# Kernel tuning notes

Measured on AMD Instinct MI355X. Metric: run time of the kernel, lower is better.

The kernel has to match this reference:

```python
import jax, jax.numpy as jnp
import numpy as np
from jax import lax

VOCAB = 50257
BEAM = 8
BSZ = 64
STEP = 16
NGRAM = 4
CAND_MULT = 2


def setup_inputs() -> dict:
    key = jax.random.key(0)
    k1, k2, k3 = jax.random.split(key, 3)
    lprobs = jax.random.normal(k1, (BSZ, BEAM, VOCAB), dtype=jnp.float32)
    scores = jax.random.normal(k2, (BSZ, BEAM, STEP), dtype=jnp.float32)
    mask = jax.random.randint(k3, (BSZ, BEAM, NGRAM), 0, 2, dtype=jnp.int32)
    return {"lprobs": lprobs, "scores": scores, "mask": mask, "step": STEP}


def reference(lprobs, scores, mask, step):
    bsz, beam_size, vocab_size = lprobs.shape
    k = CAND_MULT * beam_size

    # mask: (b, beam, n_gram) -> keep beam only if all n_gram entries nonzero
    # (original repeats over vocab then sums; summing first is equivalent and
    # avoids materializing the (b, beam, vocab, n_gram) tensor)
    n_gram = mask.shape[-1]
    keep = jnp.sum(mask, axis=-1) == n_gram  # (b, beam) bool
    lprobs = jnp.where(keep[:, :, None], lprobs, 0.0)

    if step == 0:
        lprobs = lprobs[:, 0:1, :]
        beam_size = 1
    else:
        # broadcast-add previous cumulative score of each beam
        lprobs = lprobs + scores[:, :, step - 1][:, :, None]

    flat = lprobs.reshape(bsz, beam_size * vocab_size)
    scores_buf, indices_flat = lax.top_k(flat, k)  # (b, k)
    beams_buf = indices_flat // vocab_size
    indices_buf = indices_flat % vocab_size
    return scores_buf, indices_buf, beams_buf
```

## Files before the change

### kernel.cpp

```cpp
#include <hip/hip_runtime.h>

#define VOCAB 50257
#define BEAM  8
#define BSZ   64
#define KSEL  16
#define CHUNK 4
#define TPB   256
#define PER   12568
#define BLKS_PER_ROW (BEAM * CHUNK)
#define NCAND (BLKS_PER_ROW * KSEL)
#define CAP   1024
#define SLOTS 13
#define EMPTY_KEY 1ull

static __device__ __forceinline__ unsigned int ord32(float f) {
    unsigned int u = __float_as_uint(f);
    return (u & 0x80000000u) ? ~u : (u | 0x80000000u);
}
static __device__ __forceinline__ float unord32(unsigned int o) {
    unsigned int u = (o & 0x80000000u) ? (o & 0x7FFFFFFFu) : ~o;
    return __uint_as_float(u);
}
static __device__ __forceinline__ unsigned long long mkkey(float v, unsigned int flat) {
    return ((unsigned long long)ord32(v) << 32) | (0xFFFFFFFFu - flat);
}
static __device__ __forceinline__ void publish(unsigned long long* p, unsigned long long k) {
    __hip_atomic_store(p, k, __ATOMIC_RELAXED, __HIP_MEMORY_SCOPE_AGENT);
}
static __device__ __forceinline__ unsigned long long poll(const unsigned long long* p) {
    return __hip_atomic_load(p, __ATOMIC_RELAXED, __HIP_MEMORY_SCOPE_AGENT);
}
static __device__ __forceinline__ bool slot_valid(unsigned long long k) {
    const unsigned int lo = (unsigned int)k;
    return (lo == 1u) || (lo >= 0xFFF00000u);
}

__global__ __launch_bounds__(TPB)
void beam_topk_fused(const float* __restrict__ lprobs,
                     const float* __restrict__ scores,
                     const int*   __restrict__ mask,
                     const int*   __restrict__ stepp,
                     unsigned long long* __restrict__ ws,
                     float* __restrict__ out)
{
    const int blk   = blockIdx.x;
    const int chunk = blk % CHUNK;
    const int beam  = (blk / CHUNK) % BEAM;
    const int b     = blk / (CHUNK * BEAM);
    const int tid   = threadIdx.x;
    const int step  = stepp[0];

    __shared__ unsigned long long tmax[TPB];
    __shared__ unsigned long long cand[CAP];
    __shared__ unsigned long long rowkeys[NCAND];
    __shared__ unsigned long long theta_s;
    __shared__ int ccount;
    __shared__ int wcnt;
    __shared__ int wid[KSEL];

    unsigned long long* okeys = ws + (size_t)blk * KSEL;
    const int  bb   = b * BEAM + beam;
    const int* m    = mask + bb * 4;
    const bool keep = (m[0] + m[1] + m[2] + m[3]) == 4;
    const float sadd  = (step == 0) ? 0.0f : scores[bb * 16 + (step - 1)];
    const bool active = (step != 0) || (beam == 0);
    const bool finisher = (beam == 0) && (chunk == 0);

    if (!active || (!keep && chunk != 0)) {
        if (tid < KSEL) publish(&okeys[tid], EMPTY_KEY);
    } else if (!keep) {
        if (tid < KSEL)
            publish(&okeys[tid], mkkey(sadd, (unsigned)(beam * VOCAB + tid)));
    } else {
        const int lo  = chunk * PER;
        const int len = ((lo + PER < VOCAB) ? PER : (VOCAB - lo));
        const float* base = lprobs + (size_t)bb * VOCAB;
        const float4* base4 = (const float4*)(base + lo);
        const unsigned int fb = (unsigned)(beam * VOCAB + lo);
        const int nv4 = (len + 3) >> 2;

        unsigned long long m0 = 0ull, m1 = 0ull, m2 = 0ull, m3 = 0ull;
        int j = tid;
        for (; j + 3 * TPB < nv4 - 1 || (j + 3 * TPB == nv4 - 1 && (len & 3) == 0);
             j += 4 * TPB) {
            const float4 v0 = base4[j];
            const float4 v1 = base4[j + TPB];
            const float4 v2 = base4[j + 2 * TPB];
            const float4 v3 = base4[j + 3 * TPB];
            unsigned long long k;
            const unsigned e0 = fb + 4u * (unsigned)j;
            const unsigned e1 = fb + 4u * (unsigned)(j + TPB);
            const unsigned e2 = fb + 4u * (unsigned)(j + 2 * TPB);
            const unsigned e3 = fb + 4u * (unsigned)(j + 3 * TPB);
            k = mkkey(v0.x + sadd, e0);     if (k > m0) m0 = k;
            k = mkkey(v0.y + sadd, e0 + 1); if (k > m0) m0 = k;
            k = mkkey(v0.z + sadd, e0 + 2); if (k > m0) m0 = k;
            k = mkkey(v0.w + sadd, e0 + 3); if (k > m0) m0 = k;
            k = mkkey(v1.x + sadd, e1);     if (k > m1) m1 = k;
            k = mkkey(v1.y + sadd, e1 + 1); if (k > m1) m1 = k;
            k = mkkey(v1.z + sadd, e1 + 2); if (k > m1) m1 = k;
            k = mkkey(v1.w + sadd, e1 + 3); if (k > m1) m1 = k;
            k = mkkey(v2.x + sadd, e2);     if (k > m2) m2 = k;
            k = mkkey(v2.y + sadd, e2 + 1); if (k > m2) m2 = k;
            k = mkkey(v2.z + sadd, e2 + 2); if (k > m2) m2 = k;
            k = mkkey(v2.w + sadd, e2 + 3); if (k > m2) m2 = k;
            k = mkkey(v3.x + sadd, e3);     if (k > m3) m3 = k;
            k = mkkey(v3.y + sadd, e3 + 1); if (k > m3) m3 = k;
            k = mkkey(v3.z + sadd, e3 + 2); if (k > m3) m3 = k;
            k = mkkey(v3.w + sadd, e3 + 3); if (k > m3) m3 = k;
        }
        for (; j < nv4; j += TPB) {
            const int e = 4 * j;
            #pragma unroll
            for (int u = 0; u < 4; ++u) {
                if (e + u < len) {
                    const unsigned long long k = mkkey(base[lo + e + u] + sadd,
                                                       fb + (unsigned)(e + u));
                    if (k > m0) m0 = k;
                }
            }
        }
        if (m1 > m0) m0 = m1;
        if (m2 > m0) m0 = m2;
        if (m3 > m0) m0 = m3;
        const unsigned long long mx = m0;

        tmax[tid] = mx;
        if (tid == 0) { ccount = 0; wcnt = 0; }
        __syncthreads();

        int r = 0;
        for (int jj = 0; jj < TPB; ++jj) r += (tmax[jj] > mx) ? 1 : 0;
        if (r == KSEL - 1) theta_s = mx;
        __syncthreads();
        const unsigned long long theta = theta_s;

        if (mx >= theta) wid[atomicAdd(&wcnt, 1)] = tid;
        __syncthreads();

        for (int t = tid; t < KSEL * SLOTS; t += TPB) {
            const int w  = wid[t / SLOTS];
            const int jj = w + (t % SLOTS) * TPB;
            if (jj < nv4) {
                const int e = 4 * jj;
                if (e + 3 < len) {
                    const float4 v = base4[jj];
                    const unsigned eb = fb + (unsigned)e;
                    unsigned long long k;
                    k = mkkey(v.x + sadd, eb);     if (k >= theta) cand[atomicAdd(&ccount,1)] = k;
                    k = mkkey(v.y + sadd, eb + 1); if (k >= theta) cand[atomicAdd(&ccount,1)] = k;
                    k = mkkey(v.z + sadd, eb + 2); if (k >= theta) cand[atomicAdd(&ccount,1)] = k;
                    k = mkkey(v.w + sadd, eb + 3); if (k >= theta) cand[atomicAdd(&ccount,1)] = k;
                } else {
                    #pragma unroll
                    for (int u = 0; u < 4; ++u) {
                        if (e + u < len) {
                            const unsigned long long k =
                                mkkey(base[lo + e + u] + sadd, fb + (unsigned)(e + u));
                            if (k >= theta) cand[atomicAdd(&ccount,1)] = k;
                        }
                    }
                }
            }
        }
        __syncthreads();
        const int n = ccount;

        for (int c = tid; c < n; c += TPB) {
            const unsigned long long k0 = cand[c];
            int rank = 0;
            for (int jj = 0; jj < n; ++jj) rank += (cand[jj] > k0) ? 1 : 0;
            if (rank < KSEL) publish(&okeys[rank], k0);
        }
    }

    if (!finisher) return;

    const unsigned long long* src = ws + (size_t)b * NCAND;
    for (int i = tid; i < NCAND; i += TPB) {
        unsigned long long k;
        for (;;) {
            k = poll(&src[i]);
            if (slot_valid(k)) break;
            __builtin_amdgcn_s_sleep(2);
        }
        rowkeys[i] = k;
    }
    __syncthreads();
    if (tid == 0) ccount = 0;
    __syncthreads();

    for (int i = tid; i < NCAND; i += TPB) {
        const unsigned long long k = rowkeys[i];
        if ((unsigned int)(k >> 32) != 0u) cand[atomicAdd(&ccount, 1)] = k;
    }
    __syncthreads();
    const int n = ccount;

    for (int c = tid; c < n; c += TPB) {
        const unsigned long long k0 = cand[c];
        int rank = 0;
        for (int jj = 0; jj < n; ++jj) rank += (cand[jj] > k0) ? 1 : 0;
        if (rank < KSEL) {
            const unsigned int flat = 0xFFFFFFFFu - (unsigned int)(k0 & 0xFFFFFFFFull);
            const float val = unord32((unsigned int)(k0 >> 32));
            const int vi = (int)(flat % VOCAB);
            const int bi = (int)(flat / VOCAB);
            out[b * KSEL + rank]                  = val;
            out[BSZ * KSEL + b * KSEL + rank]     = (float)vi;
            out[2 * BSZ * KSEL + b * KSEL + rank] = (float)bi;
        }
    }
}

extern "C" void kernel_launch(void* const* d_in, const int* in_sizes, int n_in,
                              void* d_out, int out_size, void* d_ws, size_t ws_size,
                              hipStream_t stream)
{
    const float* lprobs = (const float*)d_in[0];
    const float* scores = (const float*)d_in[1];
    const int*   mask   = (const int*)d_in[2];
    const int*   stepp  = (const int*)d_in[3];
    float* out = (float*)d_out;
    unsigned long long* ws = (unsigned long long*)d_ws;

    hipLaunchKernelGGL(beam_topk_fused, dim3(BSZ * BEAM * CHUNK), dim3(TPB), 0, stream,
                       lprobs, scores, mask, stepp, ws, out);
}
```

Baseline: 145.5 us.

## Halve block size and fully unroll per-thread max scan with float compares

Cuts threads per block from 256 to 128 and scales the second-pass slot count and candidate capacity to match. The max-finding pass now issues all 24 float4 loads at once, then does cheap float compares that track only a local index, and builds the 64-bit key four times at the end instead of once per element. The aim is more memory-level parallelism and less 64-bit integer work in the hot loop. In exchange it raises register pressure (24 float4 values live at once) and doubles the serial work each thread does in the rank and candidate stages.

Measured after the change: 144.0 us. No clear change (-1.0%).

```diff
diff --git a/kernel.cpp b/kernel.cpp
--- a/kernel.cpp
+++ b/kernel.cpp
@@ -5,12 +5,12 @@
 #define BSZ   64
 #define KSEL  16
 #define CHUNK 4
-#define TPB   256
+#define TPB   128
 #define PER   12568
 #define BLKS_PER_ROW (BEAM * CHUNK)
 #define NCAND (BLKS_PER_ROW * KSEL)
-#define CAP   1024
-#define SLOTS 13
+#define SLOTS 25
+#define CAP   1600
 #define EMPTY_KEY 1ull
 
 static __device__ __forceinline__ unsigned int ord32(float f) {
@@ -35,7 +35,7 @@
     return (lo == 1u) || (lo >= 0xFFF00000u);
 }
 
-__global__ __launch_bounds__(TPB)
+__global__ __launch_bounds__(TPB, 4)
 void beam_topk_fused(const float* __restrict__ lprobs,
                      const float* __restrict__ scores,
                      const int*   __restrict__ mask,
@@ -79,57 +79,71 @@
         const unsigned int fb = (unsigned)(beam * VOCAB + lo);
         const int nv4 = (len + 3) >> 2;
 
-        unsigned long long m0 = 0ull, m1 = 0ull, m2 = 0ull, m3 = 0ull;
-        int j = tid;
-        for (; j + 3 * TPB < nv4 - 1 || (j + 3 * TPB == nv4 - 1 && (len & 3) == 0);
-             j += 4 * TPB) {
-            const float4 v0 = base4[j];
-            const float4 v1 = base4[j + TPB];
-            const float4 v2 = base4[j + 2 * TPB];
-            const float4 v3 = base4[j + 3 * TPB];
-            unsigned long long k;
-            const unsigned e0 = fb + 4u * (unsigned)j;
-            const unsigned e1 = fb + 4u * (unsigned)(j + TPB);
-            const unsigned e2 = fb + 4u * (unsigned)(j + 2 * TPB);
-            const unsigned e3 = fb + 4u * (unsigned)(j + 3 * TPB);
-            k = mkkey(v0.x + sadd, e0);     if (k > m0) m0 = k;
-            k = mkkey(v0.y + sadd, e0 + 1); if (k > m0) m0 = k;
-            k = mkkey(v0.z + sadd, e0 + 2); if (k > m0) m0 = k;
-            k = mkkey(v0.w + sadd, e0 + 3); if (k > m0) m0 = k;
-            k = mkkey(v1.x + sadd, e1);     if (k > m1) m1 = k;
-            k = mkkey(v1.y + sadd, e1 + 1); if (k > m1) m1 = k;
-            k = mkkey(v1.z + sadd, e1 + 2); if (k > m1) m1 = k;
-            k = mkkey(v1.w + sadd, e1 + 3); if (k > m1) m1 = k;
-            k = mkkey(v2.x + sadd, e2);     if (k > m2) m2 = k;
-            k = mkkey(v2.y + sadd, e2 + 1); if (k > m2) m2 = k;
-            k = mkkey(v2.z + sadd, e2 + 2); if (k > m2) m2 = k;
-            k = mkkey(v2.w + sadd, e2 + 3); if (k > m2) m2 = k;
-            k = mkkey(v3.x + sadd, e3);     if (k > m3) m3 = k;
-            k = mkkey(v3.y + sadd, e3 + 1); if (k > m3) m3 = k;
-            k = mkkey(v3.z + sadd, e3 + 2); if (k > m3) m3 = k;
-            k = mkkey(v3.w + sadd, e3 + 3); if (k > m3) m3 = k;
-        }
-        for (; j < nv4; j += TPB) {
-            const int e = 4 * j;
-            #pragma unroll
-            for (int u = 0; u < 4; ++u) {
-                if (e + u < len) {
-                    const unsigned long long k = mkkey(base[lo + e + u] + sadd,
-                                                       fb + (unsigned)(e + u));
-                    if (k > m0) m0 = k;
+        float af0 = -INFINITY, af1 = -INFINITY, af2 = -INFINITY, af3 = -INFINITY;
+        int   ac0 = 0, ac1 = 0, ac2 = 0, ac3 = 0;
+
+#define LD(s) const float4 v##s = base4[tid + (s) * TPB];
+        LD(0)  LD(1)  LD(2)  LD(3)  LD(4)  LD(5)  LD(6)  LD(7)  LD(8)  LD(9)  LD(10) LD(11)
+        LD(12) LD(13) LD(14) LD(15) LD(16) LD(17) LD(18) LD(19) LD(20) LD(21) LD(22) LD(23)
+#undef LD
+
+#define R4(s, CH)                                                                   \
+        { float f;                                                                  \
+          f = v##s.x + sadd; if (f > af##CH) { af##CH = f; ac##CH = (((s) >> 2) << 2);     } \
+          f = v##s.y + sadd; if (f > af##CH) { af##CH = f; ac##CH = (((s) >> 2) << 2) + 1; } \
+          f = v##s.z + sadd; if (f > af##CH) { af##CH = f; ac##CH = (((s) >> 2) << 2) + 2; } \
+          f = v##s.w + sadd; if (f > af##CH) { af##CH = f; ac##CH = (((s) >> 2) << 2) + 3; } }
+        R4(0, 0)  R4(1, 1)  R4(2, 2)  R4(3, 3)
+        R4(4, 0)  R4(5, 1)  R4(6, 2)  R4(7, 3)
+        R4(8, 0)  R4(9, 1)  R4(10, 2) R4(11, 3)
+        R4(12, 0) R4(13, 1) R4(14, 2) R4(15, 3)
+        R4(16, 0) R4(17, 1) R4(18, 2) R4(19, 3)
+        R4(20, 0) R4(21, 1) R4(22, 2) R4(23, 3)
+#undef R4
+
+        {
+            const int j = tid + 24 * TPB;
+            if (j < nv4) {
+                const int e = 4 * j;
+                if (e + 3 < len) {
+                    const float4 v = base4[j];
+                    float f;
+                    f = v.x + sadd; if (f > af0) { af0 = f; ac0 = 24; }
+                    f = v.y + sadd; if (f > af0) { af0 = f; ac0 = 25; }
+                    f = v.z + sadd; if (f > af0) { af0 = f; ac0 = 26; }
+                    f = v.w + sadd; if (f > af0) { af0 = f; ac0 = 27; }
+                } else {
+                    #pragma unroll
+                    for (int u = 0; u < 4; ++u) {
+                        if (e + u < len) {
+                            const float f = base[lo + e + u] + sadd;
+                            if (f > af0) { af0 = f; ac0 = 24 + u; }
+                        }
+                    }
                 }
             }
         }
-        if (m1 > m0) m0 = m1;
-        if (m2 > m0) m0 = m2;
-        if (m3 > m0) m0 = m3;
-        const unsigned long long mx = m0;
+
+        const unsigned bf = fb + 4u * (unsigned)tid;
+        const unsigned long long k0 =
+            mkkey(af0, bf + 2048u * (unsigned)(ac0 >> 2)          + (unsigned)(ac0 & 3));
+        const unsigned long long k1 =
+            mkkey(af1, bf + 2048u * (unsigned)(ac1 >> 2) +  512u  + (unsigned)(ac1 & 3));
+        const unsigned long long k2 =
+            mkkey(af2, bf + 2048u * (unsigned)(ac2 >> 2) + 1024u  + (unsigned)(ac2 & 3));
+        const unsigned long long k3 =
+            mkkey(af3, bf + 2048u * (unsigned)(ac3 >> 2) + 1536u  + (unsigned)(ac3 & 3));
+        unsigned long long mx = k0;
+        if (k1 > mx) mx = k1;
+        if (k2 > mx) mx = k2;
+        if (k3 > mx) mx = k3;
 
         tmax[tid] = mx;
         if (tid == 0) { ccount = 0; wcnt = 0; }
         __syncthreads();
 
         int r = 0;
+        #pragma unroll 8
         for (int jj = 0; jj < TPB; ++jj) r += (tmax[jj] > mx) ? 1 : 0;
         if (r == KSEL - 1) theta_s = mx;
         __syncthreads();
@@ -167,10 +181,10 @@
         const int n = ccount;
 
         for (int c = tid; c < n; c += TPB) {
-            const unsigned long long k0 = cand[c];
+            const unsigned long long kc = cand[c];
             int rank = 0;
-            for (int jj = 0; jj < n; ++jj) rank += (cand[jj] > k0) ? 1 : 0;
-            if (rank < KSEL) publish(&okeys[rank], k0);
+            for (int jj = 0; jj < n; ++jj) rank += (cand[jj] > kc) ? 1 : 0;
+            if (rank < KSEL) publish(&okeys[rank], kc);
         }
     }
 
@@ -198,12 +212,12 @@
     const int n = ccount;
 
     for (int c = tid; c < n; c += TPB) {
-        const unsigned long long k0 = cand[c];
+        const unsigned long long k0c = cand[c];
         int rank = 0;
-        for (int jj = 0; jj < n; ++jj) rank += (cand[jj] > k0) ? 1 : 0;
+        for (int jj = 0; jj < n; ++jj) rank += (cand[jj] > k0c) ? 1 : 0;
         if (rank < KSEL) {
-            const unsigned int flat = 0xFFFFFFFFu - (unsigned int)(k0 & 0xFFFFFFFFull);
-            const float val = unord32((unsigned int)(k0 >> 32));
+            const unsigned int flat = 0xFFFFFFFFu - (unsigned int)(k0c & 0xFFFFFFFFull);
+            const float val = unord32((unsigned int)(k0c >> 32));
             const int vi = (int)(flat % VOCAB);
             const int bi = (int)(flat / VOCAB);
             out[b * KSEL + rank]                  = val;
```
